# Kernel optimization log

Measured on AMD Instinct MI355X. Metric: run time of the kernel, lower is better.

## Reference

```python
import jax, jax.numpy as jnp
import numpy as np

N_NODES = 100000


def sage_conv(x, src, dst, Wl, Wr, b):
    # mean-aggregate neighbor (source) features onto destinations
    msg = x[src]                                              # [E, F]
    agg = jax.ops.segment_sum(msg, dst, num_segments=N_NODES)  # [N, F]
    deg = jax.ops.segment_sum(jnp.ones(dst.shape, x.dtype), dst, num_segments=N_NODES)
    agg = agg / jnp.maximum(deg, 1.0)[:, None]
    # PyG SAGEConv: lin_l(aggr) + lin_r(x); bias only on lin_l
    return agg @ Wl.T + x @ Wr.T + b


def setup_inputs() -> dict:
    key = jax.random.key(0)
    ks = jax.random.split(key, 12)
    d, h, c = 128, 128, 6
    s = 1.0 / np.sqrt(d)
    return {
        "x": jax.random.normal(ks[0], (N_NODES, d), jnp.float32),
        "edge_index": jax.random.randint(ks[1], (2, 3200000), 0, N_NODES, jnp.int64),
        "Wl1": jax.random.normal(ks[2], (h, d), jnp.float32) * s,
        "Wr1": jax.random.normal(ks[3], (h, d), jnp.float32) * s,
        "b1": jax.random.normal(ks[4], (h,), jnp.float32) * s,
        "Wl2": jax.random.normal(ks[5], (h, h), jnp.float32) * s,
        "Wr2": jax.random.normal(ks[6], (h, h), jnp.float32) * s,
        "b2": jax.random.normal(ks[7], (h,), jnp.float32) * s,
        "Wl3": jax.random.normal(ks[8], (c, h), jnp.float32) * s,
        "Wr3": jax.random.normal(ks[9], (c, h), jnp.float32) * s,
        "b3": jax.random.normal(ks[10], (c,), jnp.float32) * s,
    }


def reference(x, edge_index, Wl1, Wr1, b1, Wl2, Wr2, b2, Wl3, Wr3, b3):
    src, dst = edge_index[0], edge_index[1]
    h = jax.nn.relu(sage_conv(x, src, dst, Wl1, Wr1, b1))  # dropout = identity (eval)
    h = jax.nn.relu(sage_conv(h, src, dst, Wl2, Wr2, b2))
    return sage_conv(h, src, dst, Wl3, Wr3, b3)  # [N, 6]
```

## Files before the change

### kernel.cpp

```cpp
#include <hip/hip_runtime.h>
#include <hip/hip_bf16.h>

#define N_NODES 100000
#define G_PART 16
#define B_PART 96
#define NPG_PAD 6272
#define A_BLOCKS 1024

__global__ __launch_bounds__(256) void partition_edges(
    const int* __restrict__ src, const int* __restrict__ dst, int E,
    int* __restrict__ bkt, unsigned int* __restrict__ gcur, int cap, int npg) {
    __shared__ int cnt16[G_PART];
    __shared__ unsigned int base16[G_PART];
    __shared__ unsigned int cur16[G_PART];
    int tid = threadIdx.x;
    if (tid < G_PART) cnt16[tid] = 0;
    __syncthreads();
    int per = (E + A_BLOCKS - 1) / A_BLOCKS;
    int beg = blockIdx.x * per;
    int end = min(beg + per, E);
    for (int i = beg + tid; i < end; i += 256) {
        int d = dst[i];
        atomicAdd(&cnt16[d / npg], 1);
    }
    __syncthreads();
    if (tid < G_PART) {
        base16[tid] = atomicAdd(&gcur[tid], (unsigned int)cnt16[tid]);
        cur16[tid] = 0;
    }
    __syncthreads();
    for (int i = beg + tid; i < end; i += 256) {
        int d = dst[i];
        int s = src[i];
        int g = d / npg;
        unsigned int p = base16[g] + atomicAdd(&cur16[g], 1u);
        bkt[(size_t)g * cap + p] = ((d - g * npg) << 17) | s;
    }
}

__global__ __launch_bounds__(256) void count_hist(const int* __restrict__ bkt,
                                                  const unsigned int* __restrict__ gcur,
                                                  int cap, int* __restrict__ partial,
                                                  int npg, int N) {
    __shared__ int hist[NPG_PAD];
    int g = blockIdx.x & (G_PART - 1);
    int b = blockIdx.x / G_PART;
    int tid = threadIdx.x;
    for (int i = tid; i < npg; i += 256) hist[i] = 0;
    __syncthreads();
    int len = (int)gcur[g];
    int per = (len + B_PART - 1) / B_PART;
    int ibeg = b * per;
    int iend = min(ibeg + per, len);
    const int* bp = bkt + (size_t)g * cap;
    for (int i = ibeg + tid; i < iend; i += 256) {
        int v = __builtin_nontemporal_load(bp + i);
        atomicAdd(&hist[v >> 17], 1);
    }
    __syncthreads();
    int base = (g * B_PART + b) * npg;
    for (int j = tid; j < npg; j += 256) partial[base + j] = hist[j];
}

__global__ __launch_bounds__(256) void scan_partials(int* __restrict__ partial,
                                                     int* __restrict__ cnt,
                                                     int npg, int N) {
    int n = blockIdx.x * 256 + threadIdx.x;
    if (n >= N) return;
    int g = n / npg;
    int i = n - g * npg;
    size_t base = (size_t)g * B_PART * npg + i;
    int run = 0;
#pragma unroll 4
    for (int b = 0; b < B_PART; ++b) {
        size_t idx = base + (size_t)b * npg;
        int t = partial[idx];
        partial[idx] = run;
        run += t;
    }
    cnt[n] = run;
}

__global__ __launch_bounds__(256) void fill_hist(const int* __restrict__ bkt,
                                                 const unsigned int* __restrict__ gcur,
                                                 int cap, const int* __restrict__ partial,
                                                 const int* __restrict__ row_off,
                                                 int* __restrict__ csr_src,
                                                 int npg, int N) {
    __shared__ int cur[NPG_PAD];
    int g = blockIdx.x & (G_PART - 1);
    int b = blockIdx.x / G_PART;
    int lo = g * npg;
    int tid = threadIdx.x;
    int pbase = (g * B_PART + b) * npg;
    for (int i = tid; i < npg && lo + i < N; i += 256)
        cur[i] = row_off[lo + i] + partial[pbase + i];
    __syncthreads();
    int len = (int)gcur[g];
    int per = (len + B_PART - 1) / B_PART;
    int ibeg = b * per;
    int iend = min(ibeg + per, len);
    const int* bp = bkt + (size_t)g * cap;
    for (int i = ibeg + tid; i < iend; i += 256) {
        int v = __builtin_nontemporal_load(bp + i);
        int p = atomicAdd(&cur[v >> 17], 1);
        csr_src[p] = v & 0x1FFFF;
    }
}

#define SCHUNK 1024

__global__ __launch_bounds__(256) void scan_blocks(const int* __restrict__ cnt,
                                                   int* __restrict__ row_off,
                                                   int* __restrict__ block_sums, int n) {
    __shared__ int ts[256];
    int tid = threadIdx.x;
    int base = blockIdx.x * SCHUNK + tid * 4;
    int v[4];
    int s = 0;
#pragma unroll
    for (int j = 0; j < 4; ++j) {
        int i = base + j;
        v[j] = (i < n) ? cnt[i] : 0;
        s += v[j];
    }
    ts[tid] = s;
    __syncthreads();
    for (int off = 1; off < 256; off <<= 1) {
        int t = 0;
        if (tid >= off) t = ts[tid - off];
        __syncthreads();
        if (tid >= off) ts[tid] += t;
        __syncthreads();
    }
    int run = (tid > 0) ? ts[tid - 1] : 0;
    if (tid == 255) block_sums[blockIdx.x] = ts[255];
#pragma unroll
    for (int j = 0; j < 4; ++j) {
        int i = base + j;
        if (i < n) row_off[i] = run;
        run += v[j];
    }
}

__global__ __launch_bounds__(256) void scan_sums(int* __restrict__ block_sums, int nb,
                                                 int* __restrict__ row_off, int n) {
    __shared__ int ts[256];
    int tid = threadIdx.x;
    int v = (tid < nb) ? block_sums[tid] : 0;
    ts[tid] = v;
    __syncthreads();
    for (int off = 1; off < 256; off <<= 1) {
        int t = 0;
        if (tid >= off) t = ts[tid - off];
        __syncthreads();
        if (tid >= off) ts[tid] += t;
        __syncthreads();
    }
    if (tid < nb) block_sums[tid] = (tid > 0) ? ts[tid - 1] : 0;
    if (tid == 255) row_off[n] = ts[255];
}

__global__ __launch_bounds__(256) void scan_add(int* __restrict__ row_off,
                                                const int* __restrict__ block_sums, int n) {
    int tid = threadIdx.x;
    int off = block_sums[blockIdx.x];
    int base = blockIdx.x * SCHUNK + tid * 4;
#pragma unroll
    for (int j = 0; j < 4; ++j) {
        int i = base + j;
        if (i < n) row_off[i] += off;
    }
}

__global__ __launch_bounds__(256) void pack_bf16(const float* __restrict__ in,
                                                 uint2* __restrict__ out, int n4) {
    int i = blockIdx.x * 256 + threadIdx.x;
    if (i >= n4) return;
    float4 v = *(const float4*)&in[(size_t)i * 4];
    __hip_bfloat162 p0 = __float22bfloat162_rn(make_float2(v.x, v.y));
    __hip_bfloat162 p1 = __float22bfloat162_rn(make_float2(v.z, v.w));
    uint2 o;
    o.x = *(const uint*)&p0;
    o.y = *(const uint*)&p1;
    out[i] = o;
}

__global__ __launch_bounds__(256) void pack_w(const float* __restrict__ Wl,
                                              const float* __restrict__ Wr,
                                              unsigned short* __restrict__ Wc) {
    int idx = blockIdx.x * 256 + threadIdx.x;
    if (idx >= 128 * 256) return;
    int n = idx >> 8, k = idx & 255;
    float v = (k < 128) ? Wl[n * 128 + k] : Wr[n * 128 + (k - 128)];
    __hip_bfloat16 b = __float2bfloat16(v);
    Wc[idx] = *(const unsigned short*)&b;
}

static __device__ inline float2 unpack2(uint v) {
    float2 r;
    r.x = __uint_as_float(v << 16);
    r.y = __uint_as_float(v & 0xffff0000u);
    return r;
}

__global__ __launch_bounds__(256) void agg_bf16(const uint* __restrict__ featb,
                                                const int* __restrict__ row_off,
                                                const int* __restrict__ csr,
                                                uint* __restrict__ outb, int M) {
    int node = blockIdx.x * 4 + (threadIdx.x >> 6);
    if (node >= M) return;
    int lane = threadIdx.x & 63;
    int beg = row_off[node], end = row_off[node + 1];
    float sx = 0.f, sy = 0.f;
    int i = beg;
    for (; i + 4 <= end; i += 4) {
        int s0 = csr[i], s1 = csr[i + 1], s2 = csr[i + 2], s3 = csr[i + 3];
        uint v0 = featb[(size_t)s0 * 64 + lane];
        uint v1 = featb[(size_t)s1 * 64 + lane];
        uint v2 = featb[(size_t)s2 * 64 + lane];
        uint v3 = featb[(size_t)s3 * 64 + lane];
        float2 f0 = unpack2(v0), f1 = unpack2(v1), f2 = unpack2(v2), f3 = unpack2(v3);
        sx += f0.x + f1.x + f2.x + f3.x;
        sy += f0.y + f1.y + f2.y + f3.y;
    }
    for (; i < end; ++i) {
        uint v = featb[(size_t)csr[i] * 64 + lane];
        float2 f = unpack2(v);
        sx += f.x;
        sy += f.y;
    }
    float inv = (end > beg) ? 1.0f / (float)(end - beg) : 0.0f;
    __hip_bfloat162 p = __float22bfloat162_rn(make_float2(sx * inv, sy * inv));
    outb[(size_t)node * 64 + lane] = *(const uint*)&p;
}

typedef __attribute__((ext_vector_type(8))) short bfrag8;
typedef __attribute__((ext_vector_type(4))) float f32x4;

__global__ __launch_bounds__(256) void gemm_mfma(
    const unsigned short* __restrict__ Aagg,
    const unsigned short* __restrict__ Aself,
    const unsigned short* __restrict__ Wc,
    const float* __restrict__ bias,
    float* __restrict__ outf,
    unsigned short* __restrict__ outb,
    int M, int relu) {
    int wave = threadIdx.x >> 6;
    int lane = threadIdx.x & 63;
    int m0 = blockIdx.x * 64 + wave * 16;
    int mrow = lane & 15;
    int quad = lane >> 4;
    int row = m0 + mrow;
    int rclamp = (row < M) ? row : 0;

    f32x4 acc[8];
#pragma unroll
    for (int t = 0; t < 8; ++t) acc[t] = (f32x4){0.f, 0.f, 0.f, 0.f};

    const unsigned short* arow0 = Aagg + (size_t)rclamp * 128;
    const unsigned short* arow1 = Aself + (size_t)rclamp * 128;
#pragma unroll
    for (int ks = 0; ks < 8; ++ks) {
        int k0 = ks * 32;
        const unsigned short* ap =
            (k0 < 128) ? (arow0 + k0 + quad * 8) : (arow1 + (k0 - 128) + quad * 8);
        bfrag8 af = *(const bfrag8*)ap;
#pragma unroll
        for (int t = 0; t < 8; ++t) {
            const unsigned short* bp = Wc + (size_t)(t * 16 + mrow) * 256 + k0 + quad * 8;
            bfrag8 bf = *(const bfrag8*)bp;
            acc[t] = __builtin_amdgcn_mfma_f32_16x16x32_bf16(af, bf, acc[t], 0, 0, 0);
        }
    }
#pragma unroll
    for (int t = 0; t < 8; ++t) {
        int col = t * 16 + mrow;
        float bcol = bias[col];
#pragma unroll
        for (int r = 0; r < 4; ++r) {
            int orow = m0 + quad * 4 + r;
            if (orow < M) {
                float v = acc[t][r] + bcol;
                if (relu) v = fmaxf(v, 0.f);
                if (outf) outf[(size_t)orow * 128 + col] = v;
                if (outb) {
                    __hip_bfloat16 hb = __float2bfloat16(v);
                    outb[(size_t)orow * 128 + col] = *(const unsigned short*)&hb;
                }
            }
        }
    }
}

__global__ __launch_bounds__(256) void lin3_kernel(const float* __restrict__ h,
                                                   const float* __restrict__ Wl,
                                                   const float* __restrict__ Wr,
                                                   const float* __restrict__ b3,
                                                   float* __restrict__ zr, int M) {
    __shared__ float Ws[12][129];
    __shared__ float hs[16][132];
    int tid = threadIdx.x;
    for (int f = tid; f < 12 * 128; f += 256) {
        int j = f >> 7, k = f & 127;
        Ws[j][k] = (j < 6) ? Wl[j * 128 + k] : Wr[(j - 6) * 128 + k];
    }
    int node0 = blockIdx.x * 16;
#pragma unroll
    for (int t = 0; t < 2; ++t) {
        int f = tid + t * 256;
        int r = f >> 5;
        int c4 = (f & 31) * 4;
        int gn = node0 + r;
        float4 v = make_float4(0.f, 0.f, 0.f, 0.f);
        if (gn < M) v = *(const float4*)&h[(size_t)gn * 128 + c4];
        *(float4*)&hs[r][c4] = v;
    }
    __syncthreads();
    int ln = tid >> 4;
    int j = tid & 15;
    int gn = node0 + ln;
    if (j < 12 && gn < M) {
        float acc = 0.f;
#pragma unroll
        for (int k = 0; k < 128; ++k) acc += hs[ln][k] * Ws[j][k];
        if (j >= 6) acc += b3[j - 6];
        zr[(size_t)gn * 12 + j] = acc;
    }
}

__global__ void out_kernel(const float* __restrict__ zr, const int* __restrict__ row_off,
                           const int* __restrict__ csr, float* __restrict__ out, int M) {
    int idx = blockIdx.x * blockDim.x + threadIdx.x;
    int node = idx >> 3;
    int j = idx & 7;
    if (node >= M || j >= 6) return;
    int beg = row_off[node], end = row_off[node + 1];
    float acc = 0.f;
    int i = beg;
    for (; i + 4 <= end; i += 4) {
        int s0 = csr[i], s1 = csr[i + 1], s2 = csr[i + 2], s3 = csr[i + 3];
        float z0 = zr[(size_t)s0 * 12 + j];
        float z1 = zr[(size_t)s1 * 12 + j];
        float z2 = zr[(size_t)s2 * 12 + j];
        float z3 = zr[(size_t)s3 * 12 + j];
        acc += z0 + z1 + z2 + z3;
    }
    for (; i < end; ++i) acc += zr[(size_t)csr[i] * 12 + j];
    float inv = (end > beg) ? 1.0f / (float)(end - beg) : 0.0f;
    out[(size_t)node * 6 + j] = acc * inv + zr[(size_t)node * 12 + 6 + j];
}

static inline size_t align_up(size_t x, size_t a) { return (x + a - 1) & ~(a - 1); }

extern "C" void kernel_launch(void* const* d_in, const int* in_sizes, int n_in,
                              void* d_out, int out_size, void* d_ws, size_t ws_size,
                              hipStream_t stream) {
    const float* x = (const float*)d_in[0];
    const int* ei = (const int*)d_in[1];
    const float* Wl1 = (const float*)d_in[2];
    const float* Wr1 = (const float*)d_in[3];
    const float* b1 = (const float*)d_in[4];
    const float* Wl2 = (const float*)d_in[5];
    const float* Wr2 = (const float*)d_in[6];
    const float* b2 = (const float*)d_in[7];
    const float* Wl3 = (const float*)d_in[8];
    const float* Wr3 = (const float*)d_in[9];
    const float* b3 = (const float*)d_in[10];

    const int N = in_sizes[0] / 128;
    const int E = in_sizes[1] / 2;
    const int* src = ei;
    const int* dst = ei + E;

    char* ws = (char*)d_ws;
    size_t off = 0;
    int* cnt = (int*)(ws + off);        off = align_up(off + (size_t)N * 4, 512);
    int* row_off = (int*)(ws + off);    off = align_up(off + (size_t)(N + 1) * 4, 512);
    int* block_sums = (int*)(ws + off); off = align_up(off + 512 * 4, 512);
    unsigned int* gcur = (unsigned int*)(ws + off); off = align_up(off + 64 * 4, 512);
    unsigned short* Wc1 = (unsigned short*)(ws + off); off = align_up(off + 128 * 256 * 2, 512);
    unsigned short* Wc2 = (unsigned short*)(ws + off); off = align_up(off + 128 * 256 * 2, 512);
    int* csr_src = (int*)(ws + off);    off = align_up(off + (size_t)E * 4, 512);
    float* slotA = (float*)(ws + off);  off = align_up(off + (size_t)N * 128 * 4, 512);
    float* slotB = (float*)(ws + off);  off = align_up(off + (size_t)N * 128 * 4, 512);
    float* h2 = (float*)(ws + off);     off = align_up(off + (size_t)N * 128 * 4, 512);
    float* zr = (float*)(ws + off);     off = align_up(off + (size_t)N * 12 * 4, 512);
    uint2* h1b = (uint2*)(ws + off);    off = align_up(off + (size_t)N * 128 * 2, 512);
    int* partial = (int*)slotA;
    uint* aggb = (uint*)slotA;
    const int cap = 210000;
    int* bkt = (int*)slotB;
    uint2* xb = (uint2*)h2;
    (void)ws_size;

    const int npg = (N + G_PART - 1) / G_PART;
    const int build_grid = G_PART * B_PART;

    hipMemsetAsync(gcur, 0, G_PART * 4, stream);
    partition_edges<<<A_BLOCKS, 256, 0, stream>>>(src, dst, E, bkt, gcur, cap, npg);
    count_hist<<<build_grid, 256, 0, stream>>>(bkt, gcur, cap, partial, npg, N);
    scan_partials<<<(N + 255) / 256, 256, 0, stream>>>(partial, cnt, npg, N);

    const int nscan = (N + SCHUNK - 1) / SCHUNK;
    scan_blocks<<<nscan, 256, 0, stream>>>(cnt, row_off, block_sums, N);
    scan_sums<<<1, 256, 0, stream>>>(block_sums, nscan, row_off, N);
    scan_add<<<nscan, 256, 0, stream>>>(row_off, block_sums, N);

    fill_hist<<<build_grid, 256, 0, stream>>>(bkt, gcur, cap, partial, row_off,
                                              csr_src, npg, N);

    const int n4 = N * 32;
    pack_bf16<<<(n4 + 255) / 256, 256, 0, stream>>>(x, xb, n4);
    pack_w<<<128, 256, 0, stream>>>(Wl1, Wr1, Wc1);
    pack_w<<<128, 256, 0, stream>>>(Wl2, Wr2, Wc2);

    int aggGrid = (N + 3) / 4;
    int gemmGrid = (N + 63) / 64;

    agg_bf16<<<aggGrid, 256, 0, stream>>>((const uint*)xb, row_off, csr_src, aggb, N);
    gemm_mfma<<<gemmGrid, 256, 0, stream>>>((const unsigned short*)aggb,
                                            (const unsigned short*)xb, Wc1, b1,
                                            nullptr, (unsigned short*)h1b, N, 1);
    agg_bf16<<<aggGrid, 256, 0, stream>>>((const uint*)h1b, row_off, csr_src, aggb, N);
    gemm_mfma<<<gemmGrid, 256, 0, stream>>>((const unsigned short*)aggb,
                                            (const unsigned short*)h1b, Wc2, b2,
                                            h2, nullptr, N, 1);
    lin3_kernel<<<(N + 15) / 16, 256, 0, stream>>>(h2, Wl3, Wr3, b3, zr, N);
    out_kernel<<<(N * 8 + 255) / 256, 256, 0, stream>>>(zr, row_off, csr_src, (float*)d_out, N);
}
```

Measured before the change: 651.2 us.

## Use bf16 for layer-3 path, MFMA lin3, 16-bit partials, merge weight packing

Layer 2 now writes bf16 output instead of fp32. The final linear layer moves from a scalar FP32 shared-memory kernel to an MFMA bf16 kernel that writes a compact 8-wide bf16 neighbor projection plus an fp32 self term. out_kernel then gathers 16-byte bf16 rows instead of 48-byte fp32 rows. The histogram partials are stored as 16-bit values to halve their traffic, and the weight packing launches are merged into one. The changes lower memory traffic and launch count at the cost of bf16 rounding in layer-3 aggregation, and they assume per-bucket counts fit in 16 bits.

Result: faster. 615.2 us (-5.5%).

```diff
diff --git a/kernel.cpp b/kernel.cpp
--- a/kernel.cpp
+++ b/kernel.cpp
@@ -40,7 +40,7 @@
 
 __global__ __launch_bounds__(256) void count_hist(const int* __restrict__ bkt,
                                                   const unsigned int* __restrict__ gcur,
-                                                  int cap, int* __restrict__ partial,
+                                                  int cap, unsigned short* __restrict__ partial,
                                                   int npg, int N) {
     __shared__ int hist[NPG_PAD];
     int g = blockIdx.x & (G_PART - 1);
@@ -58,11 +58,11 @@
         atomicAdd(&hist[v >> 17], 1);
     }
     __syncthreads();
-    int base = (g * B_PART + b) * npg;
-    for (int j = tid; j < npg; j += 256) partial[base + j] = hist[j];
-}
-
-__global__ __launch_bounds__(256) void scan_partials(int* __restrict__ partial,
+    size_t base = (size_t)(g * B_PART + b) * npg;
+    for (int j = tid; j < npg; j += 256) partial[base + j] = (unsigned short)hist[j];
+}
+
+__global__ __launch_bounds__(256) void scan_partials(unsigned short* __restrict__ partial,
                                                      int* __restrict__ cnt,
                                                      int npg, int N) {
     int n = blockIdx.x * 256 + threadIdx.x;
@@ -75,7 +75,7 @@
     for (int b = 0; b < B_PART; ++b) {
         size_t idx = base + (size_t)b * npg;
         int t = partial[idx];
-        partial[idx] = run;
+        partial[idx] = (unsigned short)run;
         run += t;
     }
     cnt[n] = run;
@@ -83,7 +83,8 @@
 
 __global__ __launch_bounds__(256) void fill_hist(const int* __restrict__ bkt,
                                                  const unsigned int* __restrict__ gcur,
-                                                 int cap, const int* __restrict__ partial,
+                                                 int cap,
+                                                 const unsigned short* __restrict__ partial,
                                                  const int* __restrict__ row_off,
                                                  int* __restrict__ csr_src,
                                                  int npg, int N) {
@@ -92,9 +93,9 @@
     int b = blockIdx.x / G_PART;
     int lo = g * npg;
     int tid = threadIdx.x;
-    int pbase = (g * B_PART + b) * npg;
+    size_t pbase = (size_t)(g * B_PART + b) * npg;
     for (int i = tid; i < npg && lo + i < N; i += 256)
-        cur[i] = row_off[lo + i] + partial[pbase + i];
+        cur[i] = row_off[lo + i] + (int)partial[pbase + i];
     __syncthreads();
     int len = (int)gcur[g];
     int per = (len + B_PART - 1) / B_PART;
@@ -186,15 +187,31 @@
     out[i] = o;
 }
 
-__global__ __launch_bounds__(256) void pack_w(const float* __restrict__ Wl,
-                                              const float* __restrict__ Wr,
-                                              unsigned short* __restrict__ Wc) {
+static __device__ inline unsigned short f2bf(float v) {
+    __hip_bfloat16 b = __float2bfloat16(v);
+    return *(const unsigned short*)&b;
+}
+
+__global__ __launch_bounds__(256) void pack_weights(
+    const float* __restrict__ Wl1, const float* __restrict__ Wr1,
+    const float* __restrict__ Wl2, const float* __restrict__ Wr2,
+    const float* __restrict__ Wl3, const float* __restrict__ Wr3,
+    unsigned short* __restrict__ Wc1, unsigned short* __restrict__ Wc2,
+    unsigned short* __restrict__ W3c) {
     int idx = blockIdx.x * 256 + threadIdx.x;
-    if (idx >= 128 * 256) return;
-    int n = idx >> 8, k = idx & 255;
-    float v = (k < 128) ? Wl[n * 128 + k] : Wr[n * 128 + (k - 128)];
-    __hip_bfloat16 b = __float2bfloat16(v);
-    Wc[idx] = *(const unsigned short*)&b;
+    if (idx < 32768) {
+        int n = idx >> 8, k = idx & 255;
+        Wc1[idx] = f2bf((k < 128) ? Wl1[n * 128 + k] : Wr1[n * 128 + (k - 128)]);
+    } else if (idx < 65536) {
+        int t = idx - 32768;
+        int n = t >> 8, k = t & 255;
+        Wc2[t] = f2bf((k < 128) ? Wl2[n * 128 + k] : Wr2[n * 128 + (k - 128)]);
+    } else if (idx < 65536 + 2048) {
+        int t = idx - 65536;
+        int n = t >> 7, k = t & 127;
+        float v = (n < 6) ? Wl3[n * 128 + k] : ((n < 12) ? Wr3[(n - 6) * 128 + k] : 0.f);
+        W3c[t] = f2bf(v);
+    }
 }
 
 static __device__ inline float2 unpack2(uint v) {
@@ -243,7 +260,6 @@
     const unsigned short* __restrict__ Aself,
     const unsigned short* __restrict__ Wc,
     const float* __restrict__ bias,
-    float* __restrict__ outf,
     unsigned short* __restrict__ outb,
     int M, int relu) {
     int wave = threadIdx.x >> 6;
@@ -283,54 +299,54 @@
             if (orow < M) {
                 float v = acc[t][r] + bcol;
                 if (relu) v = fmaxf(v, 0.f);
-                if (outf) outf[(size_t)orow * 128 + col] = v;
-                if (outb) {
-                    __hip_bfloat16 hb = __float2bfloat16(v);
-                    outb[(size_t)orow * 128 + col] = *(const unsigned short*)&hb;
-                }
+                outb[(size_t)orow * 128 + col] = f2bf(v);
             }
         }
     }
 }
 
-__global__ __launch_bounds__(256) void lin3_kernel(const float* __restrict__ h,
-                                                   const float* __restrict__ Wl,
-                                                   const float* __restrict__ Wr,
-                                                   const float* __restrict__ b3,
-                                                   float* __restrict__ zr, int M) {
-    __shared__ float Ws[12][129];
-    __shared__ float hs[16][132];
-    int tid = threadIdx.x;
-    for (int f = tid; f < 12 * 128; f += 256) {
-        int j = f >> 7, k = f & 127;
-        Ws[j][k] = (j < 6) ? Wl[j * 128 + k] : Wr[(j - 6) * 128 + k];
-    }
-    int node0 = blockIdx.x * 16;
-#pragma unroll
-    for (int t = 0; t < 2; ++t) {
-        int f = tid + t * 256;
-        int r = f >> 5;
-        int c4 = (f & 31) * 4;
-        int gn = node0 + r;
-        float4 v = make_float4(0.f, 0.f, 0.f, 0.f);
-        if (gn < M) v = *(const float4*)&h[(size_t)gn * 128 + c4];
-        *(float4*)&hs[r][c4] = v;
-    }
-    __syncthreads();
-    int ln = tid >> 4;
-    int j = tid & 15;
-    int gn = node0 + ln;
-    if (j < 12 && gn < M) {
-        float acc = 0.f;
-#pragma unroll
-        for (int k = 0; k < 128; ++k) acc += hs[ln][k] * Ws[j][k];
-        if (j >= 6) acc += b3[j - 6];
-        zr[(size_t)gn * 12 + j] = acc;
-    }
-}
-
-__global__ void out_kernel(const float* __restrict__ zr, const int* __restrict__ row_off,
-                           const int* __restrict__ csr, float* __restrict__ out, int M) {
+__global__ __launch_bounds__(256) void lin3_mfma(
+    const unsigned short* __restrict__ h2b,
+    const unsigned short* __restrict__ W3c,
+    const float* __restrict__ b3,
+    unsigned short* __restrict__ zg,
+    float* __restrict__ zs,
+    int M) {
+    int wave = threadIdx.x >> 6;
+    int lane = threadIdx.x & 63;
+    int m0 = blockIdx.x * 64 + wave * 16;
+    int mrow = lane & 15;
+    int quad = lane >> 4;
+    int row = m0 + mrow;
+    int rclamp = (row < M) ? row : 0;
+    f32x4 acc = (f32x4){0.f, 0.f, 0.f, 0.f};
+    const unsigned short* arow = h2b + (size_t)rclamp * 128;
+#pragma unroll
+    for (int ks = 0; ks < 4; ++ks) {
+        bfrag8 af = *(const bfrag8*)(arow + ks * 32 + quad * 8);
+        bfrag8 bf = *(const bfrag8*)(W3c + (size_t)mrow * 128 + ks * 32 + quad * 8);
+        acc = __builtin_amdgcn_mfma_f32_16x16x32_bf16(af, bf, acc, 0, 0, 0);
+    }
+    int col = mrow;
+#pragma unroll
+    for (int r = 0; r < 4; ++r) {
+        int orow = m0 + quad * 4 + r;
+        if (orow < M) {
+            float v = acc[r];
+            if (col < 6) {
+                zg[(size_t)orow * 8 + col] = f2bf(v);
+            } else if (col < 12) {
+                zs[(size_t)orow * 6 + (col - 6)] = v + b3[col - 6];
+            }
+        }
+    }
+}
+
+__global__ void out_kernel(const unsigned short* __restrict__ zg,
+                           const float* __restrict__ zs,
+                           const int* __restrict__ row_off,
+                           const int* __restrict__ csr,
+                           float* __restrict__ out, int M) {
     int idx = blockIdx.x * blockDim.x + threadIdx.x;
     int node = idx >> 3;
     int j = idx & 7;
@@ -340,15 +356,19 @@
     int i = beg;
     for (; i + 4 <= end; i += 4) {
         int s0 = csr[i], s1 = csr[i + 1], s2 = csr[i + 2], s3 = csr[i + 3];
-        float z0 = zr[(size_t)s0 * 12 + j];
-        float z1 = zr[(size_t)s1 * 12 + j];
-        float z2 = zr[(size_t)s2 * 12 + j];
-        float z3 = zr[(size_t)s3 * 12 + j];
-        acc += z0 + z1 + z2 + z3;
-    }
-    for (; i < end; ++i) acc += zr[(size_t)csr[i] * 12 + j];
+        uint z0 = zg[(size_t)s0 * 8 + j];
+        uint z1 = zg[(size_t)s1 * 8 + j];
+        uint z2 = zg[(size_t)s2 * 8 + j];
+        uint z3 = zg[(size_t)s3 * 8 + j];
+        acc += __uint_as_float(z0 << 16) + __uint_as_float(z1 << 16) +
+               __uint_as_float(z2 << 16) + __uint_as_float(z3 << 16);
+    }
+    for (; i < end; ++i) {
+        uint z = zg[(size_t)csr[i] * 8 + j];
+        acc += __uint_as_float(z << 16);
+    }
     float inv = (end > beg) ? 1.0f / (float)(end - beg) : 0.0f;
-    out[(size_t)node * 6 + j] = acc * inv + zr[(size_t)node * 12 + 6 + j];
+    out[(size_t)node * 6 + j] = acc * inv + zs[(size_t)node * 6 + j];
 }
 
 static inline size_t align_up(size_t x, size_t a) { return (x + a - 1) & ~(a - 1); }
@@ -381,17 +401,20 @@
     unsigned int* gcur = (unsigned int*)(ws + off); off = align_up(off + 64 * 4, 512);
     unsigned short* Wc1 = (unsigned short*)(ws + off); off = align_up(off + 128 * 256 * 2, 512);
     unsigned short* Wc2 = (unsigned short*)(ws + off); off = align_up(off + 128 * 256 * 2, 512);
+    unsigned short* W3c = (unsigned short*)(ws + off); off = align_up(off + 16 * 128 * 2, 512);
     int* csr_src = (int*)(ws + off);    off = align_up(off + (size_t)E * 4, 512);
     float* slotA = (float*)(ws + off);  off = align_up(off + (size_t)N * 128 * 4, 512);
     float* slotB = (float*)(ws + off);  off = align_up(off + (size_t)N * 128 * 4, 512);
-    float* h2 = (float*)(ws + off);     off = align_up(off + (size_t)N * 128 * 4, 512);
-    float* zr = (float*)(ws + off);     off = align_up(off + (size_t)N * 12 * 4, 512);
+    float* slotC = (float*)(ws + off);  off = align_up(off + (size_t)N * 128 * 4, 512);
     uint2* h1b = (uint2*)(ws + off);    off = align_up(off + (size_t)N * 128 * 2, 512);
-    int* partial = (int*)slotA;
+    unsigned short* partial = (unsigned short*)slotA;
     uint* aggb = (uint*)slotA;
     const int cap = 210000;
     int* bkt = (int*)slotB;
-    uint2* xb = (uint2*)h2;
+    unsigned short* h2b = (unsigned short*)slotB;
+    uint2* xb = (uint2*)slotC;
+    unsigned short* zg = (unsigned short*)slotC;
+    float* zs = (float*)((char*)slotC + align_up((size_t)N * 8 * 2, 512));
     (void)ws_size;
 
     const int npg = (N + G_PART - 1) / G_PART;
@@ -412,8 +435,8 @@
 
     const int n4 = N * 32;
     pack_bf16<<<(n4 + 255) / 256, 256, 0, stream>>>(x, xb, n4);
-    pack_w<<<128, 256, 0, stream>>>(Wl1, Wr1, Wc1);
-    pack_w<<<128, 256, 0, stream>>>(Wl2, Wr2, Wc2);
+    pack_weights<<<(65536 + 2048 + 255) / 256, 256, 0, stream>>>(
+        Wl1, Wr1, Wl2, Wr2, Wl3, Wr3, Wc1, Wc2, W3c);
 
     int aggGrid = (N + 3) / 4;
     int gemmGrid = (N + 63) / 64;
@@ -421,11 +444,12 @@
     agg_bf16<<<aggGrid, 256, 0, stream>>>((const uint*)xb, row_off, csr_src, aggb, N);
     gemm_mfma<<<gemmGrid, 256, 0, stream>>>((const unsigned short*)aggb,
                                             (const unsigned short*)xb, Wc1, b1,
-                                            nullptr, (unsigned short*)h1b, N, 1);
+                                            (unsigned short*)h1b, N, 1);
     agg_bf16<<<aggGrid, 256, 0, stream>>>((const uint*)h1b, row_off, csr_src, aggb, N);
     gemm_mfma<<<gemmGrid, 256, 0, stream>>>((const unsigned short*)aggb,
                                             (const unsigned short*)h1b, Wc2, b2,
-                                            h2, nullptr, N, 1);
-    lin3_kernel<<<(N + 15) / 16, 256, 0, stream>>>(h2, Wl3, Wr3, b3, zr, N);
-    out_kernel<<<(N * 8 + 255) / 256, 256, 0, stream>>>(zr, row_off, csr_src, (float*)d_out, N);
-}
+                                            h2b, N, 1);
+    lin3_mfma<<<gemmGrid, 256, 0, stream>>>(h2b, W3c, b3, zg, zs, N);
+    out_kernel<<<(N * 8 + 255) / 256, 256, 0, stream>>>(zg, zs, row_off, csr_src,
+                                                        (float*)d_out, N);
+}
```
